# Kernel optimization log

Measured on AMD Instinct MI355X. Metric: run time of the kernel, lower is better.

The kernel has to match this reference:

```python
import jax, jax.numpy as jnp
import numpy as np
from jax import lax

RES = [8, 12, 20, 18, 32]
C = 4            # n_features
NCELLS = 2
DOMAIN = (0.0, 1.0, 0.0, 1.0)
NPTS = 1000000


def depthwise_conv3x3(a, w):
    # a: (Ncells, C, R, R); w: (C, 1, 3, 3) depthwise (groups=C), padding=1, no bias
    return lax.conv_general_dilated(
        a, w, window_strides=(1, 1), padding='SAME',
        dimension_numbers=('NCHW', 'OIHW', 'NCHW'), feature_group_count=C)


def grid_sample_2d(feat, gx, gy):
    # Custom bilinear grid sample with per-cell half-cell offsets (offset=True).
    # feat: (Ncells, C, IH, IW); gx, gy: (N,) normalized coords in [-1, 1].
    n_cells, c, ih, iw = feat.shape
    ix = (gx + 1.0) * 0.5 * (iw - 1)          # pixel coords, align_corners=True
    iy = (gy + 1.0) * 0.5 * (ih - 1)
    off = jnp.arange(n_cells, dtype=feat.dtype) / n_cells  # staggered cells
    ix = ix[None, :] + off[:, None]            # (Ncells, N)
    iy = iy[None, :] + off[:, None]
    ix0 = jnp.floor(ix)
    iy0 = jnp.floor(iy)
    wx = ix - ix0                              # fractional weights (unclamped)
    wy = iy - iy0
    x0 = jnp.clip(ix0.astype(jnp.int32), 0, iw - 1)
    x1 = jnp.clip(ix0.astype(jnp.int32) + 1, 0, iw - 1)
    y0 = jnp.clip(iy0.astype(jnp.int32), 0, ih - 1)
    y1 = jnp.clip(iy0.astype(jnp.int32) + 1, 0, ih - 1)
    flat = feat.reshape(n_cells, c, ih * iw)

    def gather(yy, xx):
        idx = yy * iw + xx                      # (Ncells, N)
        return jnp.take_along_axis(flat, idx[:, None, :], axis=2)  # (Ncells, C, N)

    nw = gather(y0, x0)
    ne = gather(y0, x1)
    sw = gather(y1, x0)
    se = gather(y1, x1)
    w_nw = ((1 - wx) * (1 - wy))[:, None, :]
    w_ne = (wx * (1 - wy))[:, None, :]
    w_sw = ((1 - wx) * wy)[:, None, :]
    w_se = (wx * wy)[:, None, :]
    return nw * w_nw + ne * w_ne + sw * w_sw + se * w_se  # (Ncells, C, N)


def encode_level(alpha, conv_w, gx, gy):
    a = jnp.tanh(depthwise_conv3x3(alpha, conv_w))
    s = grid_sample_2d(a, gx, gy)               # (Ncells, C, N)
    return s.sum(0).T                           # (N, C) == F.sum(0).view(C,-1).t()


def setup_inputs() -> dict:
    key = jax.random.key(0)
    kx, ky, kw = jax.random.split(key, 3)
    inp = {
        'x': jax.random.uniform(kx, (NPTS, 1), dtype=jnp.float32),
        'y': jax.random.uniform(ky, (NPTS, 1), dtype=jnp.float32),
        'conv_w': jax.random.normal(kw, (C, 1, 3, 3), dtype=jnp.float32) * 0.3,
    }
    for i, r in enumerate(RES):
        inp[f'F{i}'] = jax.random.uniform(
            jax.random.fold_in(key, i + 10), (NCELLS, C, r, r),
            dtype=jnp.float32, minval=-1e-5, maxval=1e-5)
    return inp


def reference(x, y, F0, F1, F2, F3, F4, conv_w):
    x_min, x_max, y_min, y_max = DOMAIN
    gx = ((x - x_min) / (x_max - x_min)) * 2.0 - 1.0   # (N,1)
    gy = ((y - y_min) / (y_max - y_min)) * 2.0 - 1.0
    gx = gx[:, 0]
    gy = gy[:, 0]
    feats = [encode_level(F, conv_w, gx, gy) for F in (F0, F1, F2, F3, F4)]
    return jnp.concatenate(feats, axis=1)              # (N, 5*C)
```

## Files before the change

### kernel.cpp

```cpp
#include <hip/hip_runtime.h>
#include <hip/hip_fp16.h>
#include <cmath>


#define NTH 512
#define PPT 2

constexpr int PTOT = 17128;
#define OFF0 0
#define OFF1 648
#define OFF2 2000
#define OFF3 5528
#define OFF4 8416

template<int R>
__device__ __forceinline__ void conv_level(const float* __restrict__ F,
                                           const float* __restrict__ w,
                                           __half* __restrict__ dst,
                                           int tid, int nth)
{
    constexpr int P = R + 1;
    const int n = 8 * P * P;
    for (int i = tid; i < n; i += nth) {
        int c    = i & 3;
        int pos  = i >> 2;
        int cell = (pos >= P * P) ? 1 : 0;
        int rem  = pos - cell * P * P;
        int py   = rem / P;
        int px   = rem - py * P;
        int yy   = min(py, R - 1);
        int xx   = min(px, R - 1);
        const float* Fc = F + (cell * 4 + c) * R * R;
        float acc = 0.f;
#pragma unroll
        for (int ky = 0; ky < 3; ++ky) {
#pragma unroll
            for (int kx = 0; kx < 3; ++kx) {
                int sy = yy + ky - 1, sx = xx + kx - 1;
                if ((unsigned)sy < (unsigned)R && (unsigned)sx < (unsigned)R)
                    acc = fmaf(w[c * 9 + ky * 3 + kx], Fc[sy * R + sx], acc);
            }
        }
        dst[(cell * P * P + py * P + px) * 4 + c] = __float2half(tanhf(acc));
    }
}

__global__ void conv_kernel(const float* __restrict__ F0, const float* __restrict__ F1,
                            const float* __restrict__ F2, const float* __restrict__ F3,
                            const float* __restrict__ F4, const float* __restrict__ w,
                            __half* __restrict__ tab)
{
    int tid = blockIdx.x * blockDim.x + threadIdx.x;
    int nth = gridDim.x * blockDim.x;
    conv_level<8 >(F0, w, tab + OFF0, tid, nth);
    conv_level<12>(F1, w, tab + OFF1, tid, nth);
    conv_level<20>(F2, w, tab + OFF2, tid, nth);
    conv_level<18>(F3, w, tab + OFF3, tid, nth);
    conv_level<32>(F4, w, tab + OFF4, tid, nth);
}

__device__ __forceinline__ float4 cvt4(uint2 raw)
{
    __half2 lo = *(__half2*)&raw.x;
    __half2 hi = *(__half2*)&raw.y;
    float2 f01 = __half22float2(lo);
    float2 f23 = __half22float2(hi);
    return make_float4(f01.x, f01.y, f23.x, f23.y);
}

template<int R>
__device__ __forceinline__ float4 sample_level(const __half* __restrict__ lt,
                                               float px, float py)
{
    constexpr int P = R + 1;
    float fx = px * (float)(R - 1);
    float fy = py * (float)(R - 1);
    float4 acc = make_float4(0.f, 0.f, 0.f, 0.f);
#pragma unroll
    for (int cell = 0; cell < 2; ++cell) {
        float ixc = fx + 0.5f * (float)cell;
        float iyc = fy + 0.5f * (float)cell;
        float fx0 = floorf(ixc);
        float fy0 = floorf(iyc);
        float wx = ixc - fx0;
        float wy = iyc - fy0;
        int ix0 = (int)fx0;
        int iy0 = (int)fy0;
        const __half* base = lt + (size_t)(cell * P * P + iy0 * P + ix0) * 4;
        uint2 t00 = *(const uint2*)(base);
        uint2 t01 = *(const uint2*)(base + 4);
        uint2 t10 = *(const uint2*)(base + P * 4);
        uint2 t11 = *(const uint2*)(base + P * 4 + 4);
        float4 nw = cvt4(t00), ne = cvt4(t01), sw = cvt4(t10), se = cvt4(t11);
        float u = 1.f - wx, v = 1.f - wy;
        float wnw = u * v, wne = wx * v, wsw = u * wy, wse = wx * wy;
        acc.x = fmaf(wnw, nw.x, acc.x); acc.x = fmaf(wne, ne.x, acc.x);
        acc.x = fmaf(wsw, sw.x, acc.x); acc.x = fmaf(wse, se.x, acc.x);
        acc.y = fmaf(wnw, nw.y, acc.y); acc.y = fmaf(wne, ne.y, acc.y);
        acc.y = fmaf(wsw, sw.y, acc.y); acc.y = fmaf(wse, se.y, acc.y);
        acc.z = fmaf(wnw, nw.z, acc.z); acc.z = fmaf(wne, ne.z, acc.z);
        acc.z = fmaf(wsw, sw.z, acc.z); acc.z = fmaf(wse, se.z, acc.z);
        acc.w = fmaf(wnw, nw.w, acc.w); acc.w = fmaf(wne, ne.w, acc.w);
        acc.w = fmaf(wsw, sw.w, acc.w); acc.w = fmaf(wse, se.w, acc.w);
    }
    return acc;
}

__device__ __forceinline__ void sample_body(const __half* lds,
                                            const float* __restrict__ x,
                                            const float* __restrict__ y,
                                            float* __restrict__ out, int npts)
{
    int p0 = blockIdx.x * (NTH * PPT) + threadIdx.x;
    float pxs[PPT], pys[PPT];
#pragma unroll
    for (int k = 0; k < PPT; ++k) {
        int p = p0 + k * NTH;
        int pc = (p < npts) ? p : 0;
        pxs[k] = x[pc];
        pys[k] = y[pc];
    }
#pragma unroll
    for (int k = 0; k < PPT; ++k) {
        int p = p0 + k * NTH;
        if (p >= npts) continue;
        float px = pxs[k];
        float py = pys[k];
        float4* op = (float4*)(out + (size_t)p * 20);
        op[0] = sample_level<8 >(lds + OFF0, px, py);
        op[1] = sample_level<12>(lds + OFF1, px, py);
        op[2] = sample_level<20>(lds + OFF2, px, py);
        op[3] = sample_level<18>(lds + OFF3, px, py);
        op[4] = sample_level<32>(lds + OFF4, px, py);
    }
}

__global__ __launch_bounds__(NTH, 8) void sample_kernel(const float* __restrict__ x,
                                                        const float* __restrict__ y,
                                                        const __half* __restrict__ tab,
                                                        float* __restrict__ out, int npts)
{
    __shared__ __align__(16) __half lds[PTOT];
    const uint4* g4 = (const uint4*)tab;
    uint4* l4 = (uint4*)lds;
    for (int i = threadIdx.x; i < PTOT * 2 / 16; i += NTH)
        l4[i] = g4[i];
    __syncthreads();
    sample_body(lds, x, y, out, npts);
}

__global__ __launch_bounds__(NTH, 4) void fused_kernel(const float* __restrict__ x,
                                                       const float* __restrict__ y,
                                                       const float* __restrict__ F0,
                                                       const float* __restrict__ F1,
                                                       const float* __restrict__ F2,
                                                       const float* __restrict__ F3,
                                                       const float* __restrict__ F4,
                                                       const float* __restrict__ w,
                                                       float* __restrict__ out, int npts)
{
    __shared__ __align__(16) __half lds[PTOT];
    conv_level<8 >(F0, w, lds + OFF0, threadIdx.x, NTH);
    conv_level<12>(F1, w, lds + OFF1, threadIdx.x, NTH);
    conv_level<20>(F2, w, lds + OFF2, threadIdx.x, NTH);
    conv_level<18>(F3, w, lds + OFF3, threadIdx.x, NTH);
    conv_level<32>(F4, w, lds + OFF4, threadIdx.x, NTH);
    __syncthreads();
    sample_body(lds, x, y, out, npts);
}

extern "C" void kernel_launch(void* const* d_in, const int* in_sizes, int n_in,
                              void* d_out, int out_size, void* d_ws, size_t ws_size,
                              hipStream_t stream)
{
    const float* x  = (const float*)d_in[0];
    const float* y  = (const float*)d_in[1];
    const float* w  = (const float*)d_in[2];
    const float* F0 = (const float*)d_in[3];
    const float* F1 = (const float*)d_in[4];
    const float* F2 = (const float*)d_in[5];
    const float* F3 = (const float*)d_in[6];
    const float* F4 = (const float*)d_in[7];
    float* out = (float*)d_out;
    int npts = in_sizes[0];

    int nb = (npts + NTH * PPT - 1) / (NTH * PPT);

    if (ws_size >= (size_t)PTOT * sizeof(__half)) {
        __half* tab = (__half*)d_ws;
        conv_kernel<<<(PTOT + 255) / 256, 256, 0, stream>>>(F0, F1, F2, F3, F4, w, tab);
        sample_kernel<<<nb, NTH, 0, stream>>>(x, y, tab, out, npts);
    } else {
        fused_kernel<<<nb, NTH, 0, stream>>>(x, y, F0, F1, F2, F3, F4, w, out, npts);
    }
}
```

Before: 126.4 us.

## Stage sample outputs through LDS for coalesced stores, retune block size

Each thread now writes its 20-float result row into a shared-memory staging buffer, and the block then copies the whole tile to global memory with contiguous float4 stores. This replaces the 80-byte-strided per-thread stores. Block size drops to 256 threads with 4 points per thread, and the sample kernel's occupancy hint falls from 8 to 4. The cost is extra LDS use (20 KB of staging plus the table) and two barriers per point batch, which may lower occupancy.

```diff
diff --git a/kernel.cpp b/kernel.cpp
--- a/kernel.cpp
+++ b/kernel.cpp
@@ -3,8 +3,8 @@
 #include <cmath>
 
 
-#define NTH 512
-#define PPT 2
+#define NTH 256
+#define PPT 4
 
 constexpr int PTOT = 17128;
 #define OFF0 0
@@ -100,53 +100,64 @@
         acc.y = fmaf(wsw, sw.y, acc.y); acc.y = fmaf(wse, se.y, acc.y);
         acc.z = fmaf(wnw, nw.z, acc.z); acc.z = fmaf(wne, ne.z, acc.z);
         acc.z = fmaf(wsw, sw.z, acc.z); acc.z = fmaf(wse, se.z, acc.z);
-        acc.w = fmaf(wnw, nw.w, acc.w); acc.w = fmaf(wne, ne.w, acc.w);
-        acc.w = fmaf(wsw, sw.w, acc.w); acc.w = fmaf(wse, se.w, acc.w);
+        acc.w = fmaf(wnw, nw.w, acc.w); acc.w = fmaf(wse, se.w, acc.w);
+        acc.w = fmaf(wsw, sw.w, acc.w); acc.w = fmaf(wne, ne.w, acc.w);
     }
     return acc;
 }
 
-__device__ __forceinline__ void sample_body(const __half* lds,
+__device__ __forceinline__ void sample_body(const __half* lds, float* stage,
                                             const float* __restrict__ x,
                                             const float* __restrict__ y,
                                             float* __restrict__ out, int npts)
 {
-    int p0 = blockIdx.x * (NTH * PPT) + threadIdx.x;
+    const int tid = threadIdx.x;
+    const int tile0 = blockIdx.x * (NTH * PPT);
+
     float pxs[PPT], pys[PPT];
 #pragma unroll
     for (int k = 0; k < PPT; ++k) {
-        int p = p0 + k * NTH;
-        int pc = (p < npts) ? p : 0;
+        int p = tile0 + k * NTH + tid;
+        int pc = min(p, npts - 1);
         pxs[k] = x[pc];
         pys[k] = y[pc];
     }
+    __syncthreads();
+
 #pragma unroll
     for (int k = 0; k < PPT; ++k) {
-        int p = p0 + k * NTH;
-        if (p >= npts) continue;
-        float px = pxs[k];
-        float py = pys[k];
-        float4* op = (float4*)(out + (size_t)p * 20);
-        op[0] = sample_level<8 >(lds + OFF0, px, py);
-        op[1] = sample_level<12>(lds + OFF1, px, py);
-        op[2] = sample_level<20>(lds + OFF2, px, py);
-        op[3] = sample_level<18>(lds + OFF3, px, py);
-        op[4] = sample_level<32>(lds + OFF4, px, py);
-    }
-}
-
-__global__ __launch_bounds__(NTH, 8) void sample_kernel(const float* __restrict__ x,
+        int base = tile0 + k * NTH;
+        if (base >= npts) break;
+        float px = pxs[k], py = pys[k];
+        float4 r0 = sample_level<8 >(lds + OFF0, px, py);
+        float4 r1 = sample_level<12>(lds + OFF1, px, py);
+        float4 r2 = sample_level<20>(lds + OFF2, px, py);
+        float4 r3 = sample_level<18>(lds + OFF3, px, py);
+        float4 r4 = sample_level<32>(lds + OFF4, px, py);
+        float4* srow = (float4*)(stage + tid * 20);
+        srow[0] = r0; srow[1] = r1; srow[2] = r2; srow[3] = r3; srow[4] = r4;
+        __syncthreads();
+        int validf4 = min(NTH, npts - base) * 5;
+        float4* dst = (float4*)(out + (size_t)base * 20);
+        const float4* s4 = (const float4*)stage;
+        for (int j = tid; j < validf4; j += NTH)
+            dst[j] = s4[j];
+        __syncthreads();
+    }
+}
+
+__global__ __launch_bounds__(NTH, 4) void sample_kernel(const float* __restrict__ x,
                                                         const float* __restrict__ y,
                                                         const __half* __restrict__ tab,
                                                         float* __restrict__ out, int npts)
 {
     __shared__ __align__(16) __half lds[PTOT];
+    __shared__ __align__(16) float  stage[NTH * 20];
     const uint4* g4 = (const uint4*)tab;
     uint4* l4 = (uint4*)lds;
     for (int i = threadIdx.x; i < PTOT * 2 / 16; i += NTH)
         l4[i] = g4[i];
-    __syncthreads();
-    sample_body(lds, x, y, out, npts);
+    sample_body(lds, stage, x, y, out, npts);
 }
 
 __global__ __launch_bounds__(NTH, 4) void fused_kernel(const float* __restrict__ x,
@@ -160,13 +171,13 @@
                                                        float* __restrict__ out, int npts)
 {
     __shared__ __align__(16) __half lds[PTOT];
+    __shared__ __align__(16) float  stage[NTH * 20];
     conv_level<8 >(F0, w, lds + OFF0, threadIdx.x, NTH);
     conv_level<12>(F1, w, lds + OFF1, threadIdx.x, NTH);
     conv_level<20>(F2, w, lds + OFF2, threadIdx.x, NTH);
     conv_level<18>(F3, w, lds + OFF3, threadIdx.x, NTH);
     conv_level<32>(F4, w, lds + OFF4, threadIdx.x, NTH);
-    __syncthreads();
-    sample_body(lds, x, y, out, npts);
+    sample_body(lds, stage, x, y, out, npts);
 }
 
 extern "C" void kernel_launch(void* const* d_in, const int* in_sizes, int n_in,
```

Result: no change. 127.6 us (+0.9%).
